# Kernel optimization log

Hardware: AMD Instinct MI355X
Metric: run time of the kernel (lower is better)

Reference implementation:

```python
import jax, jax.numpy as jnp
import numpy as np

B, N, NQ, D, H = 16, 1024, 1024, 512, 8
HD = D // H  # per-head kq dim and per-head v-output dim (64)


def setup_inputs() -> dict:
    key = jax.random.key(0)
    ks = jax.random.split(key, 7)
    s = 0.02  # small init like torch Linear default scale
    return {
        "x":   jax.random.normal(ks[0], (B, N, D), jnp.float32),
        "r":   jax.random.normal(ks[1], (B, N, D), jnp.float32),
        "x_q": jax.random.normal(ks[2], (B, NQ, D), jnp.float32),
        # per-head projection weights, torch Linear layout (out, in), stacked over heads
        "Wq": jax.random.normal(ks[3], (H, HD, D), jnp.float32) * s,
        "Wk": jax.random.normal(ks[4], (H, HD, D), jnp.float32) * s,
        "Wv": jax.random.normal(ks[5], (H, HD, D), jnp.float32) * s,  # applied AFTER attention
        "Wo": jax.random.normal(ks[6], (D, D), jnp.float32) * s,
    }


def reference(x, r, x_q, Wq, Wk, Wv, Wo):
    # AttentionAggregator.forward(x, r, x_q) -> MultiHeadAttention(q=x_q, k=x, v=r)
    qh = jnp.einsum('bnd,hed->bhne', x_q, Wq)            # (B,H,NQ,HD)
    kh = jnp.einsum('bmd,hed->bhme', x, Wk)              # (B,H,N,HD)
    scale = jnp.sqrt(jnp.float32(HD))                    # sqrt(d_k) with d_k = head_kq_dim_out
    scores = jnp.einsum('bhne,bhme->bhnm', qh, kh) / scale
    attn = jax.nn.softmax(scores, axis=-1)               # normalize=True path
    # NOTE: v (=r) is NOT projected before attention in the original module
    ctx = jnp.einsum('bhnm,bmd->bhnd', attn, r)          # (B,H,NQ,D)
    heads = jnp.einsum('bhnd,hed->bhne', ctx, Wv)        # (B,H,NQ,HD), per-head post-projection
    concat = heads.transpose(0, 2, 1, 3).reshape(B, NQ, H * HD)  # cat over heads, dim=-1
    return concat @ Wo.T                                 # head_o (post_process=True)
```

## Files before the change

kernel.cpp:

```cpp
#include <hip/hip_runtime.h>


#define B_  16
#define N_  1024
#define D_  512
#define M_  (B_ * N_)

typedef short short8 __attribute__((ext_vector_type(8)));
typedef float f32x4 __attribute__((ext_vector_type(4)));
typedef unsigned short ushort;
typedef unsigned int uint;

__device__ __forceinline__ ushort bf16rne(float f) {
  uint u = __float_as_uint(f);
  u += 0x7FFFu + ((u >> 16) & 1u);
  return (ushort)(u >> 16);
}
__device__ __forceinline__ uint bf16pk(float lo, float hi) {
  return (uint)bf16rne(lo) | ((uint)bf16rne(hi) << 16);
}
__device__ __forceinline__ void gload_lds16(const void* g, void* l) {
  __builtin_amdgcn_global_load_lds(
      (const __attribute__((address_space(1))) uint*)g,
      (__attribute__((address_space(3))) uint*)l, 16, 0, 0);
}
__device__ __forceinline__ float exp2_hw(float x) {
  float r;
  asm("v_exp_f32 %0, %1" : "=v"(r) : "v"(x));
  return r;
}
__device__ __forceinline__ uint cvtpk_bf16(float lo, float hi) {
  uint r;
  asm("v_cvt_pk_bf16_f32 %0, %1, %2" : "=v"(r) : "v"(lo), "v"(hi));
  return r;
}

union U4S8 { uint u[4]; short8 s; };

__global__ __launch_bounds__(256) void castW_k(
    const float* __restrict__ w0, const float* __restrict__ w1,
    const float* __restrict__ w2, const float* __restrict__ w3,
    ushort* __restrict__ d, long n)
{
  const int z = blockIdx.y;
  const float* s = (z == 0) ? w0 : (z == 1) ? w1 : (z == 2) ? w2 : w3;
  const float sc = (z == 0) ? 0.1803368801f : 1.f;
  ushort* dz = d + (long)z * n;
  long i = ((long)blockIdx.x * 256 + threadIdx.x) * 8;
  float4 v0 = *(const float4*)(s + i);
  float4 v1 = *(const float4*)(s + i + 4);
  uint4 o;
  o.x = bf16pk(v0.x * sc, v0.y * sc); o.y = bf16pk(v0.z * sc, v0.w * sc);
  o.z = bf16pk(v1.x * sc, v1.y * sc); o.w = bf16pk(v1.z * sc, v1.w * sc);
  *(uint4*)(dz + i) = o;
}

template <int MODE>
__global__ __launch_bounds__(256) void gemm_k(
    const float* __restrict__ Af0, const float* __restrict__ Af1,
    const float* __restrict__ Af2, const ushort* __restrict__ Abf,
    const ushort* __restrict__ Wbase, void* __restrict__ C0,
    ushort* __restrict__ Vt)
{
  const long SB = (long)M_ * D_, WB = (long)D_ * D_;
  const int nwg = gridDim.x, per = nwg >> 3;
  const int wg = ((int)blockIdx.x & 7) * per + ((int)blockIdx.x >> 3);
  int z, bx, by;
  if constexpr (MODE == 0) { z = wg >> 9; bx = wg & 3; by = (wg & 511) >> 2; }
  else                     { z = 0;       bx = wg & 3; by = wg >> 2; }
  const ushort* W = (MODE == 0) ? Wbase + z * WB : Wbase;

  __shared__ __align__(16) ushort Bl[2][128 * 64];
  const int t = threadIdx.x, lane = t & 63, w = t >> 6;
  const int g = lane >> 4, lr = lane & 15;
  const int wr = w >> 1, wc = w & 1;
  const long m0 = (long)by * 128, n0 = (long)bx * 128;

  f32x4 acc[4][4] = {};

  auto LOADW = [&](int k0, int bufi) {
    #pragma unroll
    for (int u = 0; u < 4; ++u) {
      const int a = t * 16 + u * 4096;
      const int row = a >> 7, ch = (a >> 4) & 7;
      const int kk = k0 + ((ch ^ (row & 7)) << 3);
      gload_lds16(W + (n0 + row) * D_ + kk, (char*)Bl[bufi] + a);
    }
  };

  auto READB = [&](int cur, short8 (&bf)[4][2]) {
    #pragma unroll
    for (int nf = 0; nf < 4; ++nf)
      #pragma unroll
      for (int ks = 0; ks < 2; ++ks) {
        const int row = wc * 64 + nf * 16 + lr;
        bf[nf][ks] = *(const short8*)((const char*)Bl[cur] + row * 128 + (((ks * 4 + g) ^ (row & 7)) << 4));
      }
  };

  if constexpr (MODE == 0) {
    const float* A = (z == 0) ? Af0 : (z == 1) ? Af1 : Af2;
    const float* Aw = A + (m0 + wr * 64 + lr) * D_;

    float4 rA[16];
    auto LOADA = [&](int k0) {
      #pragma unroll
      for (int mf = 0; mf < 4; ++mf)
        #pragma unroll
        for (int ks = 0; ks < 2; ++ks) {
          const float* p = Aw + (long)mf * 16 * D_ + k0 + ks * 32 + g * 8;
          rA[mf * 4 + ks * 2 + 0] = *(const float4*)p;
          rA[mf * 4 + ks * 2 + 1] = *(const float4*)(p + 4);
        }
    };
    auto CVTA = [&](short8 (&af)[4][2]) {
      #pragma unroll
      for (int mf = 0; mf < 4; ++mf)
        #pragma unroll
        for (int ks = 0; ks < 2; ++ks) {
          const float4 a0 = rA[mf * 4 + ks * 2 + 0];
          const float4 a1 = rA[mf * 4 + ks * 2 + 1];
          U4S8 u;
          u.u[0] = cvtpk_bf16(a0.x, a0.y); u.u[1] = cvtpk_bf16(a0.z, a0.w);
          u.u[2] = cvtpk_bf16(a1.x, a1.y); u.u[3] = cvtpk_bf16(a1.z, a1.w);
          af[mf][ks] = u.s;
        }
    };

    LOADA(0);
    LOADW(0, 0);
    LOADW(64, 1);

    #pragma unroll
    for (int it = 0; it < 8; ++it) {
      const int cur = it & 1;
      if (it < 7) asm volatile("s_waitcnt vmcnt(4)" ::: "memory");
      else        asm volatile("s_waitcnt vmcnt(0)" ::: "memory");
      __builtin_amdgcn_s_barrier();

      short8 af[4][2], bf[4][2];
      CVTA(af);
      if (it + 1 < 8) LOADA((it + 1) * 64);
      READB(cur, bf);

      #pragma unroll
      for (int mf = 0; mf < 4; ++mf)
        #pragma unroll
        for (int nf = 0; nf < 4; ++nf)
          #pragma unroll
          for (int ks = 0; ks < 2; ++ks)
            acc[mf][nf] = __builtin_amdgcn_mfma_f32_16x16x32_bf16(
                af[mf][ks], bf[nf][ks], acc[mf][nf], 0, 0, 0);

      asm volatile("s_waitcnt lgkmcnt(0)" ::: "memory");
      __builtin_amdgcn_s_barrier();
      if (it + 2 < 8) LOADW((it + 2) * 64, cur);
    }
  } else {
    const ushort* A = Abf;
    __shared__ __align__(16) ushort Al[2][128 * 64];
    auto STAGE = [&](int k0, int bufi) {
      #pragma unroll
      for (int u = 0; u < 4; ++u) {
        const int a = t * 16 + u * 4096;
        const int row = a >> 7, ch = (a >> 4) & 7;
        const int kk = k0 + ((ch ^ (row & 7)) << 3);
        gload_lds16(A + (m0 + row) * D_ + kk, (char*)Al[bufi] + a);
        gload_lds16(W + (n0 + row) * D_ + kk, (char*)Bl[bufi] + a);
      }
    };
    STAGE(0, 0);
    STAGE(64, 1);
    #pragma unroll
    for (int it = 0; it < 8; ++it) {
      const int cur = it & 1;
      if (it < 7) asm volatile("s_waitcnt vmcnt(8)" ::: "memory");
      else        asm volatile("s_waitcnt vmcnt(0)" ::: "memory");
      __builtin_amdgcn_s_barrier();
      short8 af[4][2], bf[4][2];
      #pragma unroll
      for (int mf = 0; mf < 4; ++mf)
        #pragma unroll
        for (int ks = 0; ks < 2; ++ks) {
          const int row = wr * 64 + mf * 16 + lr;
          af[mf][ks] = *(const short8*)((const char*)Al[cur] + row * 128 + (((ks * 4 + g) ^ (row & 7)) << 4));
        }
      READB(cur, bf);
      #pragma unroll
      for (int mf = 0; mf < 4; ++mf)
        #pragma unroll
        for (int nf = 0; nf < 4; ++nf)
          #pragma unroll
          for (int ks = 0; ks < 2; ++ks)
            acc[mf][nf] = __builtin_amdgcn_mfma_f32_16x16x32_bf16(
                af[mf][ks], bf[nf][ks], acc[mf][nf], 0, 0, 0);
      asm volatile("s_waitcnt lgkmcnt(0)" ::: "memory");
      __builtin_amdgcn_s_barrier();
      if (it < 6) STAGE((it + 2) * 64, cur);
    }
  }

  if constexpr (MODE == 1) {
    float* C = (float*)C0;
    #pragma unroll
    for (int mf = 0; mf < 4; ++mf)
      #pragma unroll
      for (int nf = 0; nf < 4; ++nf)
        #pragma unroll
        for (int r = 0; r < 4; ++r)
          C[(m0 + wr * 64 + mf * 16 + g * 4 + r) * D_ + n0 + wc * 64 + nf * 16 + lr] =
              acc[mf][nf][r];
  } else {
    if (z < 2) {
      ushort* C = (ushort*)C0 + z * SB;
      #pragma unroll
      for (int mf = 0; mf < 4; ++mf)
        #pragma unroll
        for (int nf = 0; nf < 4; ++nf)
          #pragma unroll
          for (int r = 0; r < 4; ++r)
            C[(m0 + wr * 64 + mf * 16 + g * 4 + r) * D_ + n0 + wc * 64 + nf * 16 + lr] =
                bf16rne(acc[mf][nf][r]);
    } else {
      const int hh = (int)(n0 >> 6) + wc;
      #pragma unroll
      for (int mf = 0; mf < 4; ++mf) {
        const long m = m0 + wr * 64 + mf * 16 + g * 4;
        const int bb = (int)(m >> 10);
        const int kv = (int)(m & 1023);
        #pragma unroll
        for (int nf = 0; nf < 4; ++nf) {
          const int c = nf * 16 + lr;
          uint2 o2;
          o2.x = cvtpk_bf16(acc[mf][nf][0], acc[mf][nf][1]);
          o2.y = cvtpk_bf16(acc[mf][nf][2], acc[mf][nf][3]);
          *(uint2*)&Vt[((long)(bb * 8 + hh) * 64 + c) * (long)N_ + kv] = o2;
        }
      }
    }
  }
}

__global__ __launch_bounds__(256) void attn_mfma(
    const ushort* __restrict__ Q, const ushort* __restrict__ K,
    const ushort* __restrict__ Vt, ushort* __restrict__ Hd)
{
  __shared__ __align__(16) ushort Kl[2][64 * 64];
  __shared__ __align__(16) ushort Vl[2][64 * 64];
  const int t = threadIdx.x, lane = t & 63, w = t >> 6;
  const int g = lane >> 4, lr = lane & 15;
  const int bid = blockIdx.x;
  const int z = bid & 127, b = z >> 3, h = z & 7;
  const int qbase = (bid >> 7) * 128 + w * 32;

  short8 qf[2][2];
  #pragma unroll
  for (int nf = 0; nf < 2; ++nf)
    #pragma unroll
    for (int ks = 0; ks < 2; ++ks)
      qf[nf][ks] = *(const short8*)(Q + (long)(b * N_ + qbase + nf * 16 + lr) * D_ + h * 64 + ks * 32 + g * 8);

  const short8 ones = {0x3F80, 0x3F80, 0x3F80, 0x3F80, 0x3F80, 0x3F80, 0x3F80, 0x3F80};

  f32x4 o[2][4] = {};
  f32x4 acc_l[2] = {};

  const ushort* Kz = K + (long)b * N_ * D_ + h * 64;
  const ushort* Vz = Vt + (long)z * 64 * N_;

  auto STAGE = [&](int kt, int bufi) {
    #pragma unroll
    for (int u = 0; u < 2; ++u) {
      const int a = t * 16 + u * 4096;
      const int row = a >> 7, ch = (a >> 4) & 7;
      const int cc = (ch ^ (row & 7)) << 3;
      gload_lds16(Kz + (long)(kt * 64 + row) * D_ + cc, (char*)Kl[bufi] + a);
      gload_lds16(Vz + (long)row * N_ + kt * 64 + cc, (char*)Vl[bufi] + a);
    }
  };

  STAGE(0, 0);
  __syncthreads();

  for (int kt = 0; kt < 16; ++kt) {
    const int cur = kt & 1;
    if (kt < 15) STAGE(kt + 1, cur ^ 1);

    f32x4 s[4][2] = {};
    __builtin_amdgcn_s_setprio(1);
    #pragma unroll
    for (int mf = 0; mf < 4; ++mf) {
      short8 kf[2];
      #pragma unroll
      for (int ks = 0; ks < 2; ++ks) {
        const int row = mf * 16 + lr;
        kf[ks] = *(const short8*)((const char*)Kl[cur] + row * 128 + (((ks * 4 + g) ^ (row & 7)) << 4));
      }
      #pragma unroll
      for (int nf = 0; nf < 2; ++nf)
        #pragma unroll
        for (int ks = 0; ks < 2; ++ks)
          s[mf][nf] = __builtin_amdgcn_mfma_f32_16x16x32_bf16(kf[ks], qf[nf][ks], s[mf][nf], 0, 0, 0);
    }
    __builtin_amdgcn_s_setprio(0);

    short8 pa[2][2];
    #pragma unroll
    for (int nf = 0; nf < 2; ++nf) {
      uint Apk[4], Bpk[4];
      #pragma unroll
      for (int mf = 0; mf < 4; ++mf) {
        const float e0 = exp2_hw(s[mf][nf][0]);
        const float e1 = exp2_hw(s[mf][nf][1]);
        const float e2 = exp2_hw(s[mf][nf][2]);
        const float e3 = exp2_hw(s[mf][nf][3]);
        Apk[mf] = cvtpk_bf16(e0, e1);
        Bpk[mf] = cvtpk_bf16(e2, e3);
      }
      asm("v_permlane32_swap_b32 %0, %1" : "+v"(Apk[0]), "+v"(Apk[1]));
      asm("v_permlane16_swap_b32 %0, %1" : "+v"(Apk[0]), "+v"(Apk[1]));
      asm("v_permlane32_swap_b32 %0, %1" : "+v"(Bpk[0]), "+v"(Bpk[1]));
      asm("v_permlane16_swap_b32 %0, %1" : "+v"(Bpk[0]), "+v"(Bpk[1]));
      asm("v_permlane32_swap_b32 %0, %1" : "+v"(Apk[2]), "+v"(Apk[3]));
      asm("v_permlane16_swap_b32 %0, %1" : "+v"(Apk[2]), "+v"(Apk[3]));
      asm("v_permlane32_swap_b32 %0, %1" : "+v"(Bpk[2]), "+v"(Bpk[3]));
      asm("v_permlane16_swap_b32 %0, %1" : "+v"(Bpk[2]), "+v"(Bpk[3]));
      U4S8 u0, u1;
      u0.u[0] = Apk[0]; u0.u[1] = Bpk[0]; u0.u[2] = Apk[1]; u0.u[3] = Bpk[1];
      u1.u[0] = Apk[2]; u1.u[1] = Bpk[2]; u1.u[2] = Apk[3]; u1.u[3] = Bpk[3];
      pa[nf][0] = u0.s;
      pa[nf][1] = u1.s;
    }

    __builtin_amdgcn_s_setprio(1);
    #pragma unroll
    for (int ks = 0; ks < 2; ++ks) {
      short8 vb[4];
      #pragma unroll
      for (int nf = 0; nf < 4; ++nf) {
        const int row = nf * 16 + lr;
        vb[nf] = *(const short8*)((const char*)Vl[cur] + row * 128 + (((ks * 4 + g) ^ (row & 7)) << 4));
      }
      #pragma unroll
      for (int mf = 0; mf < 2; ++mf) {
        #pragma unroll
        for (int nf = 0; nf < 4; ++nf)
          o[mf][nf] = __builtin_amdgcn_mfma_f32_16x16x32_bf16(pa[mf][ks], vb[nf], o[mf][nf], 0, 0, 0);
        acc_l[mf] = __builtin_amdgcn_mfma_f32_16x16x32_bf16(pa[mf][ks], ones, acc_l[mf], 0, 0, 0);
      }
    }
    __builtin_amdgcn_s_setprio(0);
    __syncthreads();
  }

  #pragma unroll
  for (int mf = 0; mf < 2; ++mf)
    #pragma unroll
    for (int r = 0; r < 4; ++r) {
      const float inv = 1.f / acc_l[mf][r];
      const long grow = (long)b * N_ + qbase + mf * 16 + g * 4 + r;
      #pragma unroll
      for (int nf = 0; nf < 4; ++nf)
        Hd[grow * D_ + h * 64 + nf * 16 + lr] = bf16rne(o[mf][nf][r] * inv);
    }
}

extern "C" void kernel_launch(void* const* d_in, const int* in_sizes, int n_in,
                              void* d_out, int out_size, void* d_ws, size_t ws_size,
                              hipStream_t stream) {
  const float* x   = (const float*)d_in[0];
  const float* r   = (const float*)d_in[1];
  const float* x_q = (const float*)d_in[2];
  const float* Wq  = (const float*)d_in[3];
  const float* Wk  = (const float*)d_in[4];
  const float* Wv  = (const float*)d_in[5];
  const float* Wo  = (const float*)d_in[6];

  const long SBe = (long)M_ * D_;
  const long WBe = (long)D_ * D_;
  ushort* Qb  = (ushort*)d_ws;
  ushort* Kb  = Qb  + SBe;
  ushort* Vtb = Kb  + SBe;
  ushort* Hdb = Vtb + SBe;
  ushort* Wqb = Hdb + SBe;

  dim3 blk(256);
  castW_k<<<dim3(128, 4), blk, 0, stream>>>(Wq, Wk, Wv, Wo, Wqb, WBe);

  gemm_k<0><<<dim3(1536), blk, 0, stream>>>(x_q, x, r, nullptr, Wqb, Qb, Vtb);

  attn_mfma<<<dim3(1024), blk, 0, stream>>>(Qb, Kb, Vtb, Hdb);

  gemm_k<1><<<dim3(512), blk, 0, stream>>>(nullptr, nullptr, nullptr, Hdb,
                                           Wqb + 3 * WBe, d_out, nullptr);
}
```

Baseline: 298.7 us.

## Stage fp32 activations through LDS via async loads in projection GEMM

In the fp32-input projection GEMM (MODE 0), activations were previously loaded into registers and converted to bf16 before the MFMAs. Now the fp32 A tile and the bf16 W tile are both brought in with async global-to-LDS loads, using swizzled layouts, a K-step of 32 and 16 double-buffered iterations. A is converted from LDS to bf16 just before the MFMAs. This drops register pressure and the exposed global latency on A, but adds twice as many barriers and more LDS traffic.

```diff
diff --git a/kernel.cpp b/kernel.cpp
--- a/kernel.cpp
+++ b/kernel.cpp
@@ -68,9 +68,7 @@
   int z, bx, by;
   if constexpr (MODE == 0) { z = wg >> 9; bx = wg & 3; by = (wg & 511) >> 2; }
   else                     { z = 0;       bx = wg & 3; by = wg >> 2; }
-  const ushort* W = (MODE == 0) ? Wbase + z * WB : Wbase;
-
-  __shared__ __align__(16) ushort Bl[2][128 * 64];
+
   const int t = threadIdx.x, lane = t & 63, w = t >> 6;
   const int g = lane >> 4, lr = lane & 15;
   const int wr = w >> 1, wc = w & 1;
@@ -78,87 +76,74 @@
 
   f32x4 acc[4][4] = {};
 
-  auto LOADW = [&](int k0, int bufi) {
-    #pragma unroll
-    for (int u = 0; u < 4; ++u) {
-      const int a = t * 16 + u * 4096;
-      const int row = a >> 7, ch = (a >> 4) & 7;
-      const int kk = k0 + ((ch ^ (row & 7)) << 3);
-      gload_lds16(W + (n0 + row) * D_ + kk, (char*)Bl[bufi] + a);
-    }
-  };
-
-  auto READB = [&](int cur, short8 (&bf)[4][2]) {
-    #pragma unroll
-    for (int nf = 0; nf < 4; ++nf)
-      #pragma unroll
-      for (int ks = 0; ks < 2; ++ks) {
-        const int row = wc * 64 + nf * 16 + lr;
-        bf[nf][ks] = *(const short8*)((const char*)Bl[cur] + row * 128 + (((ks * 4 + g) ^ (row & 7)) << 4));
-      }
-  };
-
   if constexpr (MODE == 0) {
     const float* A = (z == 0) ? Af0 : (z == 1) ? Af1 : Af2;
-    const float* Aw = A + (m0 + wr * 64 + lr) * D_;
-
-    float4 rA[16];
-    auto LOADA = [&](int k0) {
+    const ushort* W = Wbase + z * WB;
+    __shared__ __align__(16) float  Afl[2][128 * 32];
+    __shared__ __align__(16) ushort Wl[2][128 * 32];
+
+    auto STAGE = [&](int k0, int bufi) {
+      #pragma unroll
+      for (int u = 0; u < 4; ++u) {
+        const int a = t * 16 + u * 4096;
+        const int row = a >> 7, ch = (a >> 4) & 7;
+        gload_lds16(A + (m0 + row) * D_ + k0 + ((ch ^ (row & 7)) << 2),
+                    (char*)Afl[bufi] + a);
+      }
+      #pragma unroll
+      for (int u = 0; u < 2; ++u) {
+        const int a = t * 16 + u * 4096;
+        const int row = a >> 6, ch = (a >> 4) & 3;
+        const int sw = (row & 3) ^ ((row >> 2) & 3);
+        gload_lds16(W + (n0 + row) * D_ + k0 + ((ch ^ sw) << 3),
+                    (char*)Wl[bufi] + a);
+      }
+    };
+
+    STAGE(0, 0);
+    STAGE(32, 1);
+
+    #pragma unroll
+    for (int it = 0; it < 16; ++it) {
+      const int cur = it & 1;
+      if (it < 15) asm volatile("s_waitcnt vmcnt(6)" ::: "memory");
+      else         asm volatile("s_waitcnt vmcnt(0)" ::: "memory");
+      __builtin_amdgcn_s_barrier();
+
+      short8 af[4], bf[4];
+      #pragma unroll
+      for (int mf = 0; mf < 4; ++mf) {
+        const int row = wr * 64 + mf * 16 + lr;
+        const int c0 = (2 * g) ^ (row & 7), c1 = (2 * g + 1) ^ (row & 7);
+        f32x4 lo = *(const f32x4*)((const char*)Afl[cur] + row * 128 + (c0 << 4));
+        f32x4 hi = *(const f32x4*)((const char*)Afl[cur] + row * 128 + (c1 << 4));
+        U4S8 u;
+        u.u[0] = cvtpk_bf16(lo[0], lo[1]); u.u[1] = cvtpk_bf16(lo[2], lo[3]);
+        u.u[2] = cvtpk_bf16(hi[0], hi[1]); u.u[3] = cvtpk_bf16(hi[2], hi[3]);
+        af[mf] = u.s;
+      }
+      #pragma unroll
+      for (int nf = 0; nf < 4; ++nf) {
+        const int row = wc * 64 + nf * 16 + lr;
+        const int sw = (row & 3) ^ ((row >> 2) & 3);
+        bf[nf] = *(const short8*)((const char*)Wl[cur] + row * 64 + ((g ^ sw) << 4));
+      }
       #pragma unroll
       for (int mf = 0; mf < 4; ++mf)
         #pragma unroll
-        for (int ks = 0; ks < 2; ++ks) {
-          const float* p = Aw + (long)mf * 16 * D_ + k0 + ks * 32 + g * 8;
-          rA[mf * 4 + ks * 2 + 0] = *(const float4*)p;
-          rA[mf * 4 + ks * 2 + 1] = *(const float4*)(p + 4);
-        }
-    };
-    auto CVTA = [&](short8 (&af)[4][2]) {
-      #pragma unroll
-      for (int mf = 0; mf < 4; ++mf)
-        #pragma unroll
-        for (int ks = 0; ks < 2; ++ks) {
-          const float4 a0 = rA[mf * 4 + ks * 2 + 0];
-          const float4 a1 = rA[mf * 4 + ks * 2 + 1];
-          U4S8 u;
-          u.u[0] = cvtpk_bf16(a0.x, a0.y); u.u[1] = cvtpk_bf16(a0.z, a0.w);
-          u.u[2] = cvtpk_bf16(a1.x, a1.y); u.u[3] = cvtpk_bf16(a1.z, a1.w);
-          af[mf][ks] = u.s;
-        }
-    };
-
-    LOADA(0);
-    LOADW(0, 0);
-    LOADW(64, 1);
-
-    #pragma unroll
-    for (int it = 0; it < 8; ++it) {
-      const int cur = it & 1;
-      if (it < 7) asm volatile("s_waitcnt vmcnt(4)" ::: "memory");
-      else        asm volatile("s_waitcnt vmcnt(0)" ::: "memory");
-      __builtin_amdgcn_s_barrier();
-
-      short8 af[4][2], bf[4][2];
-      CVTA(af);
-      if (it + 1 < 8) LOADA((it + 1) * 64);
-      READB(cur, bf);
-
-      #pragma unroll
-      for (int mf = 0; mf < 4; ++mf)
-        #pragma unroll
         for (int nf = 0; nf < 4; ++nf)
-          #pragma unroll
-          for (int ks = 0; ks < 2; ++ks)
-            acc[mf][nf] = __builtin_amdgcn_mfma_f32_16x16x32_bf16(
-                af[mf][ks], bf[nf][ks], acc[mf][nf], 0, 0, 0);
+          acc[mf][nf] = __builtin_amdgcn_mfma_f32_16x16x32_bf16(
+              af[mf], bf[nf], acc[mf][nf], 0, 0, 0);
 
       asm volatile("s_waitcnt lgkmcnt(0)" ::: "memory");
       __builtin_amdgcn_s_barrier();
-      if (it + 2 < 8) LOADW((it + 2) * 64, cur);
+      if (it + 2 < 16) STAGE((it + 2) * 32, cur);
     }
   } else {
     const ushort* A = Abf;
+    const ushort* W = Wbase;
     __shared__ __align__(16) ushort Al[2][128 * 64];
+    __shared__ __align__(16) ushort Bl[2][128 * 64];
     auto STAGE = [&](int k0, int bufi) {
       #pragma unroll
       for (int u = 0; u < 4; ++u) {
@@ -182,10 +167,11 @@
       for (int mf = 0; mf < 4; ++mf)
         #pragma unroll
         for (int ks = 0; ks < 2; ++ks) {
-          const int row = wr * 64 + mf * 16 + lr;
+          int row = wr * 64 + mf * 16 + lr;
           af[mf][ks] = *(const short8*)((const char*)Al[cur] + row * 128 + (((ks * 4 + g) ^ (row & 7)) << 4));
+          row = wc * 64 + mf * 16 + lr;
+          bf[mf][ks] = *(const short8*)((const char*)Bl[cur] + row * 128 + (((ks * 4 + g) ^ (row & 7)) << 4));
         }
-      READB(cur, bf);
       #pragma unroll
       for (int mf = 0; mf < 4; ++mf)
         #pragma unroll
```

Measured after the change: 246.0 us. 17.6% less time.
